# Kernel optimization log

Hardware: AMD Instinct MI355X
Metric: run time of the kernel (lower is better)

The kernel has to match this reference:

```python
import math
import jax, jax.numpy as jnp
import numpy as np

N_HEAD = 16
BLOCK_SIZE = 2048


def setup_inputs() -> dict:
    key = jax.random.key(0)
    ks = jax.random.split(key, 6)
    B, L, D = 2, 2048, 1024
    hs = D // N_HEAD
    s = 0.02
    return {
        "x": jax.random.normal(ks[0], (B, L, D), dtype=jnp.float32),
        "Wqkv": jax.random.normal(ks[1], (D, 3 * D), dtype=jnp.float32) * s,
        "bqkv": jax.random.normal(ks[2], (3 * D,), dtype=jnp.float32) * s,
        "Wproj": jax.random.normal(ks[3], (D, D), dtype=jnp.float32) * s,
        "bproj": jax.random.normal(ks[4], (D,), dtype=jnp.float32) * s,
        "Er": jax.random.normal(ks[5], (BLOCK_SIZE, hs), dtype=jnp.float32),
    }


def _skew(QEr):
    # QEr: [B, H, L, L] -> pad one zero column on the left, reshape, drop first row
    B, H, R, C = QEr.shape
    padded = jnp.pad(QEr, ((0, 0), (0, 0), (0, 0), (1, 0)))  # [B,H,R,C+1]
    reshaped = padded.reshape(B, H, C + 1, R)
    return reshaped[:, :, 1:, :]  # [B,H,R,C]


def reference(x, Wqkv, bqkv, Wproj, bproj, Er):
    B, L, D = x.shape
    H = N_HEAD
    hs = D // H
    qkv = x @ Wqkv + bqkv  # [B,L,3D]
    q, k, v = jnp.split(qkv, 3, axis=-1)
    q = q.reshape(B, L, H, hs).transpose(0, 2, 1, 3)  # [B,H,L,hs]
    k = k.reshape(B, L, H, hs).transpose(0, 2, 1, 3)
    v = v.reshape(B, L, H, hs).transpose(0, 2, 1, 3)

    Er_used = Er[BLOCK_SIZE - L:, :]           # [L, hs]
    QEr = jnp.einsum('bhld,md->bhlm', q, Er_used)  # q @ Er^T -> [B,H,L,L]
    Srel = _skew(QEr)

    scale = 1.0 / math.sqrt(hs)
    att = (jnp.einsum('bhld,bhmd->bhlm', q, k) + Srel) * scale
    causal = jnp.tril(jnp.ones((L, L), dtype=bool))
    att = jnp.where(causal[None, None], att, -jnp.inf)
    att = jax.nn.softmax(att, axis=-1)
    y = jnp.einsum('bhlm,bhmd->bhld', att, v)  # [B,H,L,hs]
    y = y.transpose(0, 2, 1, 3).reshape(B, L, D)
    return y @ Wproj + bproj
```

## Files before the change

kernel.cpp:

```cpp
#include <hip/hip_runtime.h>
#include <hip/hip_bf16.h>

#define LSEQ 2048
#define NH 16
#define HS 64
#define DIM 1024

typedef __attribute__((ext_vector_type(8))) short short8;
typedef __attribute__((ext_vector_type(4))) float f32x4;

typedef const __attribute__((address_space(1))) void g_void_t;
typedef __attribute__((address_space(3))) void s_void_t;

static __device__ __forceinline__ short f2bf(float f) {
  __hip_bfloat16 h = __float2bfloat16(f);
  return __builtin_bit_cast(short, h);
}


__global__ void cast_kernel(const float* __restrict__ in, short* __restrict__ out, int n4) {
  int i = blockIdx.x * blockDim.x + threadIdx.x;
  if (i < n4) {
    float4 v = reinterpret_cast<const float4*>(in)[i];
    short4 o;
    o.x = f2bf(v.x); o.y = f2bf(v.y); o.z = f2bf(v.z); o.w = f2bf(v.w);
    reinterpret_cast<short4*>(out)[i] = o;
  }
}

__global__ void transpose_cast_kernel(const float* __restrict__ W, short* __restrict__ Wt,
                                      int K, int N) {
  __shared__ float tile[64][65];
  int k0 = blockIdx.y * 64, n0 = blockIdx.x * 64;
  int t = threadIdx.x;
  int r4 = t >> 6, cc = t & 63;
  for (int i = 0; i < 16; ++i) {
    int row = i * 4 + r4;
    tile[row][cc] = W[(size_t)(k0 + row) * N + (n0 + cc)];
  }
  __syncthreads();
  for (int i = 0; i < 16; ++i) {
    int row = i * 4 + r4;
    Wt[(size_t)(n0 + row) * K + (k0 + cc)] = f2bf(tile[cc][row]);
  }
}

__global__ void transpose_v_kernel(const short* __restrict__ V, short* __restrict__ Vt) {
  __shared__ short tile[64][65];
  int bh = blockIdx.y;
  int l0 = blockIdx.x * 64;
  int t = threadIdx.x;
  const short* src = V + ((size_t)bh * LSEQ + l0) * HS;
  for (int i = 0; i < 2; ++i) {
    int ch = i * 256 + t;
    int row = ch >> 3, c8 = ch & 7;
    uint4 v = *reinterpret_cast<const uint4*>(src + row * HS + c8 * 8);
    short tmp[8];
    *reinterpret_cast<uint4*>(tmp) = v;
#pragma unroll
    for (int e = 0; e < 8; ++e) tile[row][c8 * 8 + e] = tmp[e];
  }
  __syncthreads();
  short* dst = Vt + (size_t)bh * HS * LSEQ + l0;
  for (int i = 0; i < 2; ++i) {
    int ch = i * 256 + t;
    int d = ch >> 3, c8 = ch & 7;
    short tmp[8];
#pragma unroll
    for (int e = 0; e < 8; ++e) tmp[e] = tile[c8 * 8 + e][d];
    *reinterpret_cast<uint4*>(dst + (size_t)d * LSEQ + c8 * 8) = *reinterpret_cast<uint4*>(tmp);
  }
}


template<int MODE>
__global__ __launch_bounds__(256, 2) void gemm_bt_kernel(
    const short* __restrict__ A, const short* __restrict__ Bt,
    const float* __restrict__ bias, int M, int N, int K,
    short* __restrict__ oq, short* __restrict__ ok, short* __restrict__ ov,
    float* __restrict__ of)
{
  __shared__ short Al[128 * 32];
  __shared__ short Bl[128 * 32];
  const int m0 = blockIdx.y * 128, n0 = blockIdx.x * 128;
  const int t = threadIdx.x;
  const int lane = t & 63, wave = t >> 6;
  const int wr = wave >> 1, wc = wave & 1;
  const int g = lane >> 4, c = lane & 15;
  f32x4 acc[4][4] = {};

  for (int k0 = 0; k0 < K; k0 += 32) {
    __syncthreads();
    for (int i = 0; i < 2; ++i) {
      int ch = i * 256 + t;
      int row = ch >> 2, c8 = ch & 3;
      __builtin_amdgcn_global_load_lds(
          (g_void_t*)(A + (size_t)(m0 + row) * K + k0 + c8 * 8),
          (s_void_t*)(Al + (i * 256 + wave * 64) * 8), 16, 0, 0);
      __builtin_amdgcn_global_load_lds(
          (g_void_t*)(Bt + (size_t)(n0 + row) * K + k0 + c8 * 8),
          (s_void_t*)(Bl + (i * 256 + wave * 64) * 8), 16, 0, 0);
    }
    __syncthreads();
    short8 af[4], bf[4];
#pragma unroll
    for (int mi = 0; mi < 4; ++mi) {
      int row = wr * 64 + mi * 16 + c;
      af[mi] = *reinterpret_cast<const short8*>(Al + row * 32 + g * 8);
    }
#pragma unroll
    for (int ni = 0; ni < 4; ++ni) {
      int row = wc * 64 + ni * 16 + c;
      bf[ni] = *reinterpret_cast<const short8*>(Bl + row * 32 + g * 8);
    }
#pragma unroll
    for (int mi = 0; mi < 4; ++mi)
#pragma unroll
      for (int ni = 0; ni < 4; ++ni)
        acc[mi][ni] = __builtin_amdgcn_mfma_f32_16x16x32_bf16(af[mi], bf[ni], acc[mi][ni], 0, 0, 0);
  }

#pragma unroll
  for (int mi = 0; mi < 4; ++mi)
#pragma unroll
    for (int ni = 0; ni < 4; ++ni) {
      int n = n0 + wc * 64 + ni * 16 + c;
      float bv = bias[n];
#pragma unroll
      for (int r = 0; r < 4; ++r) {
        int m = m0 + wr * 64 + mi * 16 + g * 4 + r;
        float val = acc[mi][ni][r] + bv;
        if (MODE == 0) {
          int which = n >> 10;
          int hh2 = (n >> 6) & 15;
          int d = n & 63;
          int b = m >> 11, ll = m & 2047;
          short* dst = which == 0 ? oq : (which == 1 ? ok : ov);
          dst[(((size_t)b * NH + hh2) * LSEQ + ll) * HS + d] = f2bf(val);
        } else {
          of[(size_t)m * N + n] = val;
        }
      }
    }
}


__global__ __launch_bounds__(256, 2) void attn_kernel(
    const short* __restrict__ Qb, const short* __restrict__ Kb,
    const short* __restrict__ VTb, const short* __restrict__ Erb,
    short* __restrict__ Y)
{
  const int bid = blockIdx.x;
  const int qt = 31 - (bid >> 5);
  const int bh = bid & 31;
  const int l0 = qt * 64;
  const int bb = bh >> 4, hh = bh & 15;
  const int t = threadIdx.x;
  const int lane = t & 63, wave = t >> 6;
  const int g = lane >> 4, c = lane & 15;
  const int r8 = lane >> 3;
  const int c16b = (lane & 7) * 16;

  __shared__ short Ql[64 * 64];
  __shared__ short Kl[2][64 * 64];
  __shared__ short Vl[2][64 * 64];
  __shared__ short El[2][128 * 64];
  __shared__ short Pl[4][16 * 64];

  const short* Qg = Qb + ((size_t)bh * LSEQ + l0) * HS;
  for (int i = 0; i < 2; ++i) {
    int ch = i * 256 + t;
    int row = ch >> 3, c8 = ch & 7;
    uint4 v = *reinterpret_cast<const uint4*>(Qg + row * HS + c8 * 8);
    int byte = row * 128 + ((c8 * 16) ^ ((row & 7) << 4));
    *reinterpret_cast<uint4*>(reinterpret_cast<char*>(Ql) + byte) = v;
  }
  __syncthreads();

  short8 qf[2];
#pragma unroll
  for (int kk = 0; kk < 2; ++kk) {
    int row = wave * 16 + c;
    int byte = row * 128 + ((kk * 32 + g * 8) * 2 ^ ((row & 7) << 4));
    qf[kk] = *reinterpret_cast<const short8*>(reinterpret_cast<char*>(Ql) + byte);
  }

  f32x4 acc_o[4] = {};
  float mrun[4], lrun[4];
#pragma unroll
  for (int r = 0; r < 4; ++r) { mrun[r] = -1e30f; lrun[r] = 0.0f; }

  const int nsteps = qt + 1;

  auto issue_stage = [&](int step, int sel) {
    const int m0 = step * 64;
    const char* Kg = (const char*)(Kb + ((size_t)bh * LSEQ + m0) * HS);
#pragma unroll
    for (int j = 0; j < 2; ++j) {
      int row = wave * 16 + j * 8 + r8;
      __builtin_amdgcn_global_load_lds(
          (g_void_t*)(Kg + row * 128 + (c16b ^ ((row & 7) << 4))),
          (s_void_t*)(&Kl[sel][(wave * 16 + j * 8) * 64]), 16, 0, 0);
    }
#pragma unroll
    for (int j = 0; j < 2; ++j) {
      int row = wave * 16 + j * 8 + r8;
      const char* Vg = (const char*)(VTb + ((size_t)bh * HS + row) * LSEQ + m0);
      __builtin_amdgcn_global_load_lds(
          (g_void_t*)(Vg + (c16b ^ ((row & 7) << 4))),
          (s_void_t*)(&Vl[sel][(wave * 16 + j * 8) * 64]), 16, 0, 0);
    }
    const int c0 = LSEQ - 1 - l0 + m0;
#pragma unroll
    for (int j = 0; j < 4; ++j) {
      int row = wave * 32 + j * 8 + r8;
      int e = c0 - 63 + row;
      e = e < 0 ? 0 : (e > LSEQ - 1 ? LSEQ - 1 : e);
      __builtin_amdgcn_global_load_lds(
          (g_void_t*)((const char*)(Erb + (size_t)e * HS) + (c16b ^ ((row & 7) << 4))),
          (s_void_t*)(&El[sel][(wave * 32 + j * 8) * 64]), 16, 0, 0);
    }
  };

  issue_stage(0, 0);

  for (int step = 0; step < nsteps; ++step) {
    const int sel = step & 1;
    const bool diag = (step == qt);

    if (step + 1 < nsteps) {
      issue_stage(step + 1, sel ^ 1);
      asm volatile("s_waitcnt vmcnt(8)" ::: "memory");
    } else {
      asm volatile("s_waitcnt vmcnt(0)" ::: "memory");
    }
    __builtin_amdgcn_s_barrier();
    __builtin_amdgcn_sched_barrier(0);

    f32x4 ga[5];
#pragma unroll
    for (int s5 = 0; s5 < 5; ++s5) {
      int nsb = (3 - wave) + s5;
      ga[s5] = (f32x4){0.0f, 0.0f, 0.0f, 0.0f};
#pragma unroll
      for (int kk = 0; kk < 2; ++kk) {
        int row = nsb * 16 + c;
        int byte = row * 128 + ((kk * 32 + g * 8) * 2 ^ ((row & 7) << 4));
        short8 ef = *reinterpret_cast<const short8*>((char*)El[sel] + byte);
        ga[s5] = __builtin_amdgcn_mfma_f32_16x16x32_bf16(qf[kk], ef, ga[s5], 0, 0, 0);
      }
    }

    f32x4 sa[4];
#pragma unroll
    for (int ns = 0; ns < 4; ++ns) {
      sa[ns] = (f32x4){0.0f, 0.0f, 0.0f, 0.0f};
#pragma unroll
      for (int kk = 0; kk < 2; ++kk) {
        int row = ns * 16 + c;
        int byte = row * 128 + ((kk * 32 + g * 8) * 2 ^ ((row & 7) << 4));
        short8 kf = *reinterpret_cast<const short8*>((char*)Kl[sel] + byte);
        sa[ns] = __builtin_amdgcn_mfma_f32_16x16x32_bf16(qf[kk], kf, sa[ns], 0, 0, 0);
      }
    }

    float sv[4][4];
#pragma unroll
    for (int r = 0; r < 4; ++r) {
      int i4 = g * 4 + r;
      int u = c + 15 - i4;
      int srcl = (g << 4) | (u & 15);
      bool lo = (u < 16);
#pragma unroll
      for (int ns = 0; ns < 4; ++ns) {
        float va = __shfl(ga[ns][r], srcl, 64);
        float vb = __shfl(ga[ns + 1][r], srcl, 64);
        float srel = lo ? va : vb;
        float x = (sa[ns][r] + srel) * 0.125f;
        if (diag && (ns * 16 + c > wave * 16 + i4)) x = -1e30f;
        sv[ns][r] = x;
      }
    }

    float mnew[4], al[4];
#pragma unroll
    for (int r = 0; r < 4; ++r) {
      float mx = fmaxf(fmaxf(sv[0][r], sv[1][r]), fmaxf(sv[2][r], sv[3][r]));
      mx = fmaxf(mx, __shfl_xor(mx, 1));
      mx = fmaxf(mx, __shfl_xor(mx, 2));
      mx = fmaxf(mx, __shfl_xor(mx, 4));
      mx = fmaxf(mx, __shfl_xor(mx, 8));
      mnew[r] = fmaxf(mrun[r], mx);
      al[r] = __expf(mrun[r] - mnew[r]);
      mrun[r] = mnew[r];
    }
#pragma unroll
    for (int ns = 0; ns < 4; ++ns)
#pragma unroll
      for (int r = 0; r < 4; ++r)
        sv[ns][r] = __expf(sv[ns][r] - mnew[r]);
#pragma unroll
    for (int r = 0; r < 4; ++r) {
      float s = sv[0][r] + sv[1][r] + sv[2][r] + sv[3][r];
      s += __shfl_xor(s, 1);
      s += __shfl_xor(s, 2);
      s += __shfl_xor(s, 4);
      s += __shfl_xor(s, 8);
      lrun[r] = lrun[r] * al[r] + s;
    }
#pragma unroll
    for (int ns = 0; ns < 4; ++ns)
#pragma unroll
      for (int r = 0; r < 4; ++r)
        acc_o[ns][r] *= al[r];

    short* Pw = Pl[wave];
#pragma unroll
    for (int ns = 0; ns < 4; ++ns)
#pragma unroll
      for (int r = 0; r < 4; ++r) {
        int row = g * 4 + r;
        int byte = row * 128 + (((ns * 16 + c) * 2) ^ ((row & 7) << 4));
        *reinterpret_cast<short*>(reinterpret_cast<char*>(Pw) + byte) = f2bf(sv[ns][r]);
      }

#pragma unroll
    for (int kk = 0; kk < 2; ++kk) {
      int kbyte = (kk * 32 + g * 8) * 2;
      int byteP = c * 128 + (kbyte ^ ((c & 7) << 4));
      short8 pf = *reinterpret_cast<const short8*>(reinterpret_cast<char*>(Pw) + byteP);
#pragma unroll
      for (int ns = 0; ns < 4; ++ns) {
        int rowV = ns * 16 + c;
        int byteV = rowV * 128 + (kbyte ^ ((rowV & 7) << 4));
        short8 vf = *reinterpret_cast<const short8*>((char*)Vl[sel] + byteV);
        acc_o[ns] = __builtin_amdgcn_mfma_f32_16x16x32_bf16(pf, vf, acc_o[ns], 0, 0, 0);
      }
    }

    __builtin_amdgcn_sched_barrier(0);
    __builtin_amdgcn_s_barrier();
  }

#pragma unroll
  for (int ns = 0; ns < 4; ++ns)
#pragma unroll
    for (int r = 0; r < 4; ++r) {
      int row = g * 4 + r;
      float inv = 1.0f / lrun[r];
      int lg = l0 + wave * 16 + row;
      int d = ns * 16 + c;
      Y[((size_t)bb * LSEQ + lg) * DIM + hh * HS + d] = f2bf(acc_o[ns][r] * inv);
    }
}


extern "C" void kernel_launch(void* const* d_in, const int* in_sizes, int n_in,
                              void* d_out, int out_size, void* d_ws, size_t ws_size,
                              hipStream_t stream)
{
  const float* x     = (const float*)d_in[0];
  const float* Wqkv  = (const float*)d_in[1];
  const float* bqkv  = (const float*)d_in[2];
  const float* Wproj = (const float*)d_in[3];
  const float* bproj = (const float*)d_in[4];
  const float* Er    = (const float*)d_in[5];

  char* ws = (char*)d_ws;
  short* xb     = (short*)(ws + 0);
  short* WqkvT  = (short*)(ws + 8388608);
  short* WprojT = (short*)(ws + 14680064);
  short* Erb    = (short*)(ws + 16777216);
  short* qB     = (short*)(ws + 17039360);
  short* kB     = (short*)(ws + 25427968);
  short* vB     = (short*)(ws + 33816576);
  short* yB     = (short*)(ws + 42205184);
  short* vT     = xb;

  cast_kernel<<<4096, 256, 0, stream>>>(x, xb, 4096 * 1024 / 4);
  cast_kernel<<<128, 256, 0, stream>>>(Er, Erb, 2048 * 64 / 4);
  transpose_cast_kernel<<<dim3(3072 / 64, 1024 / 64), 256, 0, stream>>>(Wqkv, WqkvT, 1024, 3072);
  transpose_cast_kernel<<<dim3(1024 / 64, 1024 / 64), 256, 0, stream>>>(Wproj, WprojT, 1024, 1024);

  gemm_bt_kernel<0><<<dim3(3072 / 128, 4096 / 128), 256, 0, stream>>>(
      xb, WqkvT, bqkv, 4096, 3072, 1024, qB, kB, vB, nullptr);

  transpose_v_kernel<<<dim3(32, 32), 256, 0, stream>>>(vB, vT);

  attn_kernel<<<dim3(1024), 256, 0, stream>>>(qB, kB, vT, Erb, yB);

  gemm_bt_kernel<1><<<dim3(1024 / 128, 4096 / 128), 256, 0, stream>>>(
      yB, WprojT, bproj, 4096, 1024, 1024, nullptr, nullptr, nullptr, (float*)d_out);
}
```

Baseline: 172.7 us.

## Pair causal query tiles per block, fold scale into Q, use exp2 and DPP reductions

Each attention block now handles two query tiles (qt and 31-qt), so every block does the same number of causal steps; the grid is halved from 1024 to 512 blocks. The softmax scale and log2(e) are folded into Q in the QKV GEMM epilogue, so the inner loop can use exp2 and skip a multiply. Row max and sum reductions switch from shuffles to DPP moves. The running-max rescale is skipped when no row's max grows by more than 4. This targets tail imbalance and softmax ALU cost, in exchange for fewer blocks in flight and slightly looser numerics from the lazy rescale.

```diff
diff --git a/kernel.cpp b/kernel.cpp
--- a/kernel.cpp
+++ b/kernel.cpp
@@ -12,9 +12,39 @@
 typedef const __attribute__((address_space(1))) void g_void_t;
 typedef __attribute__((address_space(3))) void s_void_t;
 
+#define QSCALE 0.18033688011112042f
+
 static __device__ __forceinline__ short f2bf(float f) {
   __hip_bfloat16 h = __float2bfloat16(f);
   return __builtin_bit_cast(short, h);
+}
+
+static __device__ __forceinline__ float fexp2(float x) {
+#if __has_builtin(__builtin_amdgcn_exp2f)
+  return __builtin_amdgcn_exp2f(x);
+#else
+  float r; asm("v_exp_f32 %0, %1" : "=v"(r) : "v"(x)); return r;
+#endif
+}
+
+template<int CTRL>
+static __device__ __forceinline__ float dpp_mov(float x) {
+  return __builtin_bit_cast(float,
+      __builtin_amdgcn_update_dpp(0, __builtin_bit_cast(int, x), CTRL, 0xF, 0xF, true));
+}
+static __device__ __forceinline__ float redmax16(float x) {
+  x = fmaxf(x, dpp_mov<0xB1>(x));
+  x = fmaxf(x, dpp_mov<0x4E>(x));
+  x = fmaxf(x, dpp_mov<0x141>(x));
+  x = fmaxf(x, dpp_mov<0x140>(x));
+  return x;
+}
+static __device__ __forceinline__ float redsum16(float x) {
+  x += dpp_mov<0xB1>(x);
+  x += dpp_mov<0x4E>(x);
+  x += dpp_mov<0x141>(x);
+  x += dpp_mov<0x140>(x);
+  return x;
 }
 
 
@@ -135,6 +165,7 @@
           int hh2 = (n >> 6) & 15;
           int d = n & 63;
           int b = m >> 11, ll = m & 2047;
+          if (which == 0) val *= QSCALE;
           short* dst = which == 0 ? oq : (which == 1 ? ok : ov);
           dst[(((size_t)b * NH + hh2) * LSEQ + ll) * HS + d] = f2bf(val);
         } else {
@@ -151,9 +182,8 @@
     short* __restrict__ Y)
 {
   const int bid = blockIdx.x;
-  const int qt = 31 - (bid >> 5);
+  const int pair = bid >> 5;
   const int bh = bid & 31;
-  const int l0 = qt * 64;
   const int bb = bh >> 4, hh = bh & 15;
   const int t = threadIdx.x;
   const int lane = t & 63, wave = t >> 6;
@@ -167,191 +197,197 @@
   __shared__ short El[2][128 * 64];
   __shared__ short Pl[4][16 * 64];
 
-  const short* Qg = Qb + ((size_t)bh * LSEQ + l0) * HS;
-  for (int i = 0; i < 2; ++i) {
-    int ch = i * 256 + t;
-    int row = ch >> 3, c8 = ch & 7;
-    uint4 v = *reinterpret_cast<const uint4*>(Qg + row * HS + c8 * 8);
-    int byte = row * 128 + ((c8 * 16) ^ ((row & 7) << 4));
-    *reinterpret_cast<uint4*>(reinterpret_cast<char*>(Ql) + byte) = v;
-  }
-  __syncthreads();
-
-  short8 qf[2];
-#pragma unroll
-  for (int kk = 0; kk < 2; ++kk) {
-    int row = wave * 16 + c;
-    int byte = row * 128 + ((kk * 32 + g * 8) * 2 ^ ((row & 7) << 4));
-    qf[kk] = *reinterpret_cast<const short8*>(reinterpret_cast<char*>(Ql) + byte);
-  }
-
-  f32x4 acc_o[4] = {};
-  float mrun[4], lrun[4];
-#pragma unroll
-  for (int r = 0; r < 4; ++r) { mrun[r] = -1e30f; lrun[r] = 0.0f; }
-
-  const int nsteps = qt + 1;
-
-  auto issue_stage = [&](int step, int sel) {
-    const int m0 = step * 64;
-    const char* Kg = (const char*)(Kb + ((size_t)bh * LSEQ + m0) * HS);
-#pragma unroll
-    for (int j = 0; j < 2; ++j) {
-      int row = wave * 16 + j * 8 + r8;
-      __builtin_amdgcn_global_load_lds(
-          (g_void_t*)(Kg + row * 128 + (c16b ^ ((row & 7) << 4))),
-          (s_void_t*)(&Kl[sel][(wave * 16 + j * 8) * 64]), 16, 0, 0);
-    }
-#pragma unroll
-    for (int j = 0; j < 2; ++j) {
-      int row = wave * 16 + j * 8 + r8;
-      const char* Vg = (const char*)(VTb + ((size_t)bh * HS + row) * LSEQ + m0);
-      __builtin_amdgcn_global_load_lds(
-          (g_void_t*)(Vg + (c16b ^ ((row & 7) << 4))),
-          (s_void_t*)(&Vl[sel][(wave * 16 + j * 8) * 64]), 16, 0, 0);
-    }
-    const int c0 = LSEQ - 1 - l0 + m0;
-#pragma unroll
-    for (int j = 0; j < 4; ++j) {
-      int row = wave * 32 + j * 8 + r8;
-      int e = c0 - 63 + row;
-      e = e < 0 ? 0 : (e > LSEQ - 1 ? LSEQ - 1 : e);
-      __builtin_amdgcn_global_load_lds(
-          (g_void_t*)((const char*)(Erb + (size_t)e * HS) + (c16b ^ ((row & 7) << 4))),
-          (s_void_t*)(&El[sel][(wave * 32 + j * 8) * 64]), 16, 0, 0);
-    }
-  };
-
-  issue_stage(0, 0);
-
-  for (int step = 0; step < nsteps; ++step) {
-    const int sel = step & 1;
-    const bool diag = (step == qt);
-
-    if (step + 1 < nsteps) {
-      issue_stage(step + 1, sel ^ 1);
-      asm volatile("s_waitcnt vmcnt(8)" ::: "memory");
-    } else {
-      asm volatile("s_waitcnt vmcnt(0)" ::: "memory");
-    }
-    __builtin_amdgcn_s_barrier();
-    __builtin_amdgcn_sched_barrier(0);
-
-    f32x4 ga[5];
-#pragma unroll
-    for (int s5 = 0; s5 < 5; ++s5) {
-      int nsb = (3 - wave) + s5;
-      ga[s5] = (f32x4){0.0f, 0.0f, 0.0f, 0.0f};
+  auto process = [&](int qt) {
+    const int l0 = qt * 64;
+
+    const short* Qg = Qb + ((size_t)bh * LSEQ + l0) * HS;
+    for (int i = 0; i < 2; ++i) {
+      int ch = i * 256 + t;
+      int row = ch >> 3, c8 = ch & 7;
+      uint4 v = *reinterpret_cast<const uint4*>(Qg + row * HS + c8 * 8);
+      int byte = row * 128 + ((c8 * 16) ^ ((row & 7) << 4));
+      *reinterpret_cast<uint4*>(reinterpret_cast<char*>(Ql) + byte) = v;
+    }
+    __syncthreads();
+
+    short8 qf[2];
+#pragma unroll
+    for (int kk = 0; kk < 2; ++kk) {
+      int row = wave * 16 + c;
+      int byte = row * 128 + ((kk * 32 + g * 8) * 2 ^ ((row & 7) << 4));
+      qf[kk] = *reinterpret_cast<const short8*>(reinterpret_cast<char*>(Ql) + byte);
+    }
+
+    f32x4 acc_o[4] = {};
+    float mrun[4], lrun[4];
+#pragma unroll
+    for (int r = 0; r < 4; ++r) { mrun[r] = -1e30f; lrun[r] = 0.0f; }
+
+    const int nsteps = qt + 1;
+
+    auto issue_stage = [&](int step, int sel) {
+      const int m0 = step * 64;
+      const char* Kg = (const char*)(Kb + ((size_t)bh * LSEQ + m0) * HS);
+#pragma unroll
+      for (int j = 0; j < 2; ++j) {
+        int row = wave * 16 + j * 8 + r8;
+        __builtin_amdgcn_global_load_lds(
+            (g_void_t*)(Kg + row * 128 + (c16b ^ ((row & 7) << 4))),
+            (s_void_t*)(&Kl[sel][(wave * 16 + j * 8) * 64]), 16, 0, 0);
+      }
+#pragma unroll
+      for (int j = 0; j < 2; ++j) {
+        int row = wave * 16 + j * 8 + r8;
+        const char* Vg = (const char*)(VTb + ((size_t)bh * HS + row) * LSEQ + m0);
+        __builtin_amdgcn_global_load_lds(
+            (g_void_t*)(Vg + (c16b ^ ((row & 7) << 4))),
+            (s_void_t*)(&Vl[sel][(wave * 16 + j * 8) * 64]), 16, 0, 0);
+      }
+      const int c0 = LSEQ - 1 - l0 + m0;
+#pragma unroll
+      for (int j = 0; j < 4; ++j) {
+        int row = wave * 32 + j * 8 + r8;
+        int e = c0 - 63 + row;
+        e = e < 0 ? 0 : (e > LSEQ - 1 ? LSEQ - 1 : e);
+        __builtin_amdgcn_global_load_lds(
+            (g_void_t*)((const char*)(Erb + (size_t)e * HS) + (c16b ^ ((row & 7) << 4))),
+            (s_void_t*)(&El[sel][(wave * 32 + j * 8) * 64]), 16, 0, 0);
+      }
+    };
+
+    issue_stage(0, 0);
+
+    for (int step = 0; step < nsteps; ++step) {
+      const int sel = step & 1;
+      const bool diag = (step == qt);
+
+      if (step + 1 < nsteps) {
+        issue_stage(step + 1, sel ^ 1);
+        asm volatile("s_waitcnt vmcnt(8)" ::: "memory");
+      } else {
+        asm volatile("s_waitcnt vmcnt(0)" ::: "memory");
+      }
+      __builtin_amdgcn_s_barrier();
+      __builtin_amdgcn_sched_barrier(0);
+
+      f32x4 ga[5];
+#pragma unroll
+      for (int s5 = 0; s5 < 5; ++s5) {
+        int nsb = (3 - wave) + s5;
+        ga[s5] = (f32x4){0.0f, 0.0f, 0.0f, 0.0f};
+#pragma unroll
+        for (int kk = 0; kk < 2; ++kk) {
+          int row = nsb * 16 + c;
+          int byte = row * 128 + ((kk * 32 + g * 8) * 2 ^ ((row & 7) << 4));
+          short8 ef = *reinterpret_cast<const short8*>((char*)El[sel] + byte);
+          ga[s5] = __builtin_amdgcn_mfma_f32_16x16x32_bf16(qf[kk], ef, ga[s5], 0, 0, 0);
+        }
+      }
+
+      f32x4 sa[4];
+#pragma unroll
+      for (int ns = 0; ns < 4; ++ns) {
+        sa[ns] = (f32x4){0.0f, 0.0f, 0.0f, 0.0f};
+#pragma unroll
+        for (int kk = 0; kk < 2; ++kk) {
+          int row = ns * 16 + c;
+          int byte = row * 128 + ((kk * 32 + g * 8) * 2 ^ ((row & 7) << 4));
+          short8 kf = *reinterpret_cast<const short8*>((char*)Kl[sel] + byte);
+          sa[ns] = __builtin_amdgcn_mfma_f32_16x16x32_bf16(qf[kk], kf, sa[ns], 0, 0, 0);
+        }
+      }
+
+      float sv[4][4];
+#pragma unroll
+      for (int r = 0; r < 4; ++r) {
+        int i4 = g * 4 + r;
+        int u0 = c + 15 - i4;
+        int srcl = (g << 4) | (u0 & 15);
+        float bp[5];
+#pragma unroll
+        for (int s5 = 0; s5 < 5; ++s5) bp[s5] = __shfl(ga[s5][r], srcl, 64);
+        bool lo = (u0 < 16);
+#pragma unroll
+        for (int ns = 0; ns < 4; ++ns) {
+          float srel = lo ? bp[ns] : bp[ns + 1];
+          float x = sa[ns][r] + srel;
+          if (diag && (ns * 16 + c > wave * 16 + i4)) x = -1e30f;
+          sv[ns][r] = x;
+        }
+      }
+
+      float mx[4];
+      bool need = false;
+#pragma unroll
+      for (int r = 0; r < 4; ++r) {
+        float m = fmaxf(fmaxf(sv[0][r], sv[1][r]), fmaxf(sv[2][r], sv[3][r]));
+        mx[r] = redmax16(m);
+        need = need || (mx[r] > mrun[r] + 4.0f);
+      }
+      if (__ballot(need)) {
+#pragma unroll
+        for (int r = 0; r < 4; ++r) {
+          float mnew = fmaxf(mrun[r], mx[r]);
+          float al = fexp2(mrun[r] - mnew);
+          mrun[r] = mnew;
+          lrun[r] *= al;
+#pragma unroll
+          for (int ns = 0; ns < 4; ++ns) acc_o[ns][r] *= al;
+        }
+      }
+#pragma unroll
+      for (int ns = 0; ns < 4; ++ns)
+#pragma unroll
+        for (int r = 0; r < 4; ++r)
+          sv[ns][r] = fexp2(sv[ns][r] - mrun[r]);
+#pragma unroll
+      for (int r = 0; r < 4; ++r) {
+        float s = (sv[0][r] + sv[1][r]) + (sv[2][r] + sv[3][r]);
+        lrun[r] += redsum16(s);
+      }
+
+      short* Pw = Pl[wave];
+#pragma unroll
+      for (int ns = 0; ns < 4; ++ns)
+#pragma unroll
+        for (int r = 0; r < 4; ++r) {
+          int row = g * 4 + r;
+          int byte = row * 128 + (((ns * 16 + c) * 2) ^ ((row & 7) << 4));
+          *reinterpret_cast<short*>(reinterpret_cast<char*>(Pw) + byte) = f2bf(sv[ns][r]);
+        }
+
 #pragma unroll
       for (int kk = 0; kk < 2; ++kk) {
-        int row = nsb * 16 + c;
-        int byte = row * 128 + ((kk * 32 + g * 8) * 2 ^ ((row & 7) << 4));
-        short8 ef = *reinterpret_cast<const short8*>((char*)El[sel] + byte);
-        ga[s5] = __builtin_amdgcn_mfma_f32_16x16x32_bf16(qf[kk], ef, ga[s5], 0, 0, 0);
-      }
-    }
-
-    f32x4 sa[4];
-#pragma unroll
-    for (int ns = 0; ns < 4; ++ns) {
-      sa[ns] = (f32x4){0.0f, 0.0f, 0.0f, 0.0f};
-#pragma unroll
-      for (int kk = 0; kk < 2; ++kk) {
-        int row = ns * 16 + c;
-        int byte = row * 128 + ((kk * 32 + g * 8) * 2 ^ ((row & 7) << 4));
-        short8 kf = *reinterpret_cast<const short8*>((char*)Kl[sel] + byte);
-        sa[ns] = __builtin_amdgcn_mfma_f32_16x16x32_bf16(qf[kk], kf, sa[ns], 0, 0, 0);
-      }
-    }
-
-    float sv[4][4];
-#pragma unroll
-    for (int r = 0; r < 4; ++r) {
-      int i4 = g * 4 + r;
-      int u = c + 15 - i4;
-      int srcl = (g << 4) | (u & 15);
-      bool lo = (u < 16);
-#pragma unroll
-      for (int ns = 0; ns < 4; ++ns) {
-        float va = __shfl(ga[ns][r], srcl, 64);
-        float vb = __shfl(ga[ns + 1][r], srcl, 64);
-        float srel = lo ? va : vb;
-        float x = (sa[ns][r] + srel) * 0.125f;
-        if (diag && (ns * 16 + c > wave * 16 + i4)) x = -1e30f;
-        sv[ns][r] = x;
-      }
-    }
-
-    float mnew[4], al[4];
-#pragma unroll
-    for (int r = 0; r < 4; ++r) {
-      float mx = fmaxf(fmaxf(sv[0][r], sv[1][r]), fmaxf(sv[2][r], sv[3][r]));
-      mx = fmaxf(mx, __shfl_xor(mx, 1));
-      mx = fmaxf(mx, __shfl_xor(mx, 2));
-      mx = fmaxf(mx, __shfl_xor(mx, 4));
-      mx = fmaxf(mx, __shfl_xor(mx, 8));
-      mnew[r] = fmaxf(mrun[r], mx);
-      al[r] = __expf(mrun[r] - mnew[r]);
-      mrun[r] = mnew[r];
-    }
-#pragma unroll
-    for (int ns = 0; ns < 4; ++ns)
-#pragma unroll
-      for (int r = 0; r < 4; ++r)
-        sv[ns][r] = __expf(sv[ns][r] - mnew[r]);
-#pragma unroll
-    for (int r = 0; r < 4; ++r) {
-      float s = sv[0][r] + sv[1][r] + sv[2][r] + sv[3][r];
-      s += __shfl_xor(s, 1);
-      s += __shfl_xor(s, 2);
-      s += __shfl_xor(s, 4);
-      s += __shfl_xor(s, 8);
-      lrun[r] = lrun[r] * al[r] + s;
-    }
-#pragma unroll
-    for (int ns = 0; ns < 4; ++ns)
-#pragma unroll
-      for (int r = 0; r < 4; ++r)
-        acc_o[ns][r] *= al[r];
-
-    short* Pw = Pl[wave];
+        int kbyte = (kk * 32 + g * 8) * 2;
+        int byteP = c * 128 + (kbyte ^ ((c & 7) << 4));
+        short8 pf = *reinterpret_cast<const short8*>(reinterpret_cast<char*>(Pw) + byteP);
+#pragma unroll
+        for (int ns = 0; ns < 4; ++ns) {
+          int rowV = ns * 16 + c;
+          int byteV = rowV * 128 + (kbyte ^ ((rowV & 7) << 4));
+          short8 vf = *reinterpret_cast<const short8*>((char*)Vl[sel] + byteV);
+          acc_o[ns] = __builtin_amdgcn_mfma_f32_16x16x32_bf16(pf, vf, acc_o[ns], 0, 0, 0);
+        }
+      }
+
+      __builtin_amdgcn_sched_barrier(0);
+      __builtin_amdgcn_s_barrier();
+    }
+
 #pragma unroll
     for (int ns = 0; ns < 4; ++ns)
 #pragma unroll
       for (int r = 0; r < 4; ++r) {
         int row = g * 4 + r;
-        int byte = row * 128 + (((ns * 16 + c) * 2) ^ ((row & 7) << 4));
-        *reinterpret_cast<short*>(reinterpret_cast<char*>(Pw) + byte) = f2bf(sv[ns][r]);
-      }
-
-#pragma unroll
-    for (int kk = 0; kk < 2; ++kk) {
-      int kbyte = (kk * 32 + g * 8) * 2;
-      int byteP = c * 128 + (kbyte ^ ((c & 7) << 4));
-      short8 pf = *reinterpret_cast<const short8*>(reinterpret_cast<char*>(Pw) + byteP);
-#pragma unroll
-      for (int ns = 0; ns < 4; ++ns) {
-        int rowV = ns * 16 + c;
-        int byteV = rowV * 128 + (kbyte ^ ((rowV & 7) << 4));
-        short8 vf = *reinterpret_cast<const short8*>((char*)Vl[sel] + byteV);
-        acc_o[ns] = __builtin_amdgcn_mfma_f32_16x16x32_bf16(pf, vf, acc_o[ns], 0, 0, 0);
-      }
-    }
-
-    __builtin_amdgcn_sched_barrier(0);
-    __builtin_amdgcn_s_barrier();
-  }
-
-#pragma unroll
-  for (int ns = 0; ns < 4; ++ns)
-#pragma unroll
-    for (int r = 0; r < 4; ++r) {
-      int row = g * 4 + r;
-      float inv = 1.0f / lrun[r];
-      int lg = l0 + wave * 16 + row;
-      int d = ns * 16 + c;
-      Y[((size_t)bb * LSEQ + lg) * DIM + hh * HS + d] = f2bf(acc_o[ns][r] * inv);
-    }
+        float inv = 1.0f / lrun[r];
+        int lg = l0 + wave * 16 + row;
+        int d = ns * 16 + c;
+        Y[((size_t)bb * LSEQ + lg) * DIM + hh * HS + d] = f2bf(acc_o[ns][r] * inv);
+      }
+  };
+
+  process(31 - pair);
+  process(pair);
 }
 
 
@@ -387,7 +423,7 @@
 
   transpose_v_kernel<<<dim3(32, 32), 256, 0, stream>>>(vB, vT);
 
-  attn_kernel<<<dim3(1024), 256, 0, stream>>>(qB, kB, vT, Erb, yB);
+  attn_kernel<<<dim3(512), 256, 0, stream>>>(qB, kB, vT, Erb, yB);
 
   gemm_bt_kernel<1><<<dim3(1024 / 128, 4096 / 128), 256, 0, stream>>>(
       yB, WprojT, bproj, 4096, 1024, 1024, nullptr, nullptr, nullptr, (float*)d_out);
```

After: 153.2 us. 11.3% less time.
